# Kernel optimization log

Measured on AMD Instinct MI355X. Metric: run time of the kernel, lower is better.

The kernel has to match this reference:

```python
import jax, jax.numpy as jnp
import numpy as np
from jax import lax

B, T, HID, NH = 4, 2048, 1024, 16
D = HID // NH
LN_EPS = 1e-5
NORM_EPS = 1e-6


def setup_inputs() -> dict:
    key = jax.random.key(0)
    ks = jax.random.split(key, 3)
    s = 0.02
    return {
        "x": jax.random.normal(ks[0], (B, T, HID), jnp.float32),
        "ln_g": jnp.ones((HID,), jnp.float32),
        "ln_b": jnp.zeros((HID,), jnp.float32),
        "w_qkvb": jax.random.normal(ks[1], (HID, 4 * HID), jnp.float32) * s,
        "b_qkvb": jnp.zeros((4 * HID,), jnp.float32),
        "w_out": jax.random.normal(ks[2], (HID, HID), jnp.float32) * s,
        "b_out": jnp.zeros((HID,), jnp.float32),
    }


def reference(x, ln_g, ln_b, w_qkvb, b_qkvb, w_out, b_out):
    b, t = x.shape[:2]
    # LayerNorm (biased variance, eps=1e-5, matching nn.LayerNorm)
    mu = jnp.mean(x, axis=-1, keepdims=True)
    var = jnp.mean((x - mu) ** 2, axis=-1, keepdims=True)
    normed = (x - mu) * lax.rsqrt(var + LN_EPS) * ln_g + ln_b

    proj = normed @ w_qkvb + b_qkvb  # [B,T,4H]
    q, k, v, beta_pre = jnp.split(proj, 4, axis=-1)
    beta = jax.nn.sigmoid(beta_pre)

    def heads(a):  # [B,T,H] -> [T,B,NH,D] (time-major for scan)
        return a.reshape(b, t, NH, D).transpose(1, 0, 2, 3)

    q, k, v, beta = heads(q), heads(k), heads(v), heads(beta)
    # F.normalize(k, dim=-1, eps=1e-6)
    k = k / jnp.maximum(jnp.linalg.norm(k, axis=-1, keepdims=True), NORM_EPS)

    S0 = jnp.zeros((b, NH, D, D), x.dtype)

    def step(S, inp):
        q_t, k_t, v_t, beta_t = inp  # each [B,NH,D]
        retrieval = jnp.einsum('bhij,bhj->bhi', S, k_t)
        S = S + jnp.einsum('bhi,bhj->bhij', beta_t * (v_t - retrieval), k_t)
        o_t = jnp.einsum('bhij,bhj->bhi', S, q_t)
        return S, o_t

    _, out_t = lax.scan(step, S0, (q, k, v, beta))  # out_t: [T,B,NH,D]
    scan_out = out_t.transpose(1, 0, 2, 3).reshape(b, t, NH * D)
    return x + scan_out @ w_out + b_out
```

## Files before the change

### kernel.cpp

```cpp
#include <hip/hip_runtime.h>
#include <hip/hip_bf16.h>

typedef __attribute__((ext_vector_type(8))) short short8;
typedef __attribute__((ext_vector_type(4))) float f32x4;

#define P72 72

__device__ __forceinline__ unsigned short f2bf(float f) {
    union { float f; unsigned int u; } v; v.f = f;
    unsigned int r = (v.u + 0x7FFFu + ((v.u >> 16) & 1u)) >> 16;
    return (unsigned short)r;
}
__device__ __forceinline__ float bf2f(unsigned short b) {
    union { unsigned int u; float f; } v; v.u = ((unsigned int)b) << 16; return v.f;
}

#define WAVE_SYNC() do { __asm__ volatile("s_waitcnt lgkmcnt(0)" ::: "memory"); \
                         __builtin_amdgcn_sched_barrier(0); } while (0)

#define LGKM_BARRIER() do { __asm__ volatile("s_waitcnt lgkmcnt(0)" ::: "memory"); \
                            __builtin_amdgcn_s_barrier(); \
                            __builtin_amdgcn_sched_barrier(0); } while (0)

#define ASYNC16(G, L) __builtin_amdgcn_global_load_lds( \
    (const __attribute__((address_space(1))) void*)(G), \
    (__attribute__((address_space(3))) void*)(L), 16, 0, 0)

__global__ __launch_bounds__(256) void ln_wqt_kernel(
    const float* __restrict__ x, const float* __restrict__ g,
    const float* __restrict__ bv_, unsigned short* __restrict__ out,
    const float* __restrict__ w_qkvb, unsigned short* __restrict__ WQT)
{
    __shared__ float pool[32 * 33];
    const int tid = threadIdx.x;
    if (blockIdx.x < 8192) {
        const int row = blockIdx.x;
        const float4 v = ((const float4*)(x + (size_t)row * 1024))[tid];
        float s  = v.x + v.y + v.z + v.w;
        float s2 = v.x * v.x + v.y * v.y + v.z * v.z + v.w * v.w;
#pragma unroll
        for (int off = 1; off < 64; off <<= 1) {
            s  += __shfl_xor(s, off);
            s2 += __shfl_xor(s2, off);
        }
        const int wv = tid >> 6;
        if ((tid & 63) == 0) { pool[wv] = s; pool[4 + wv] = s2; }
        __syncthreads();
        s  = pool[0] + pool[1] + pool[2] + pool[3];
        s2 = pool[4] + pool[5] + pool[6] + pool[7];
        const float mu  = s * (1.0f / 1024.0f);
        const float var = s2 * (1.0f / 1024.0f) - mu * mu;
        const float inv = rsqrtf(var + 1e-5f);
        const float4 gv = ((const float4*)g)[tid];
        const float4 bb = ((const float4*)bv_)[tid];
        ushort4 o;
        o.x = f2bf((v.x - mu) * inv * gv.x + bb.x);
        o.y = f2bf((v.y - mu) * inv * gv.y + bb.y);
        o.z = f2bf((v.z - mu) * inv * gv.z + bb.z);
        o.w = f2bf((v.w - mu) * inv * gv.w + bb.w);
        *(ushort4*)(out + (size_t)row * 1024 + tid * 4) = o;
    } else {
        const int blk = blockIdx.x - 8192;
        const int c0 = (blk & 127) * 32, r0 = (blk >> 7) * 32;
        const int tx = tid & 31, ty = tid >> 5;
#pragma unroll
        for (int yy = 0; yy < 32; yy += 8)
            pool[(ty + yy) * 33 + tx] = w_qkvb[(size_t)(r0 + ty + yy) * 4096 + c0 + tx];
        __syncthreads();
#pragma unroll
        for (int yy = 0; yy < 32; yy += 8)
            WQT[(size_t)(c0 + ty + yy) * 1024 + r0 + tx] = f2bf(pool[tx * 33 + ty + yy]);
    }
}

__global__ __launch_bounds__(256) void gemm128(
    const unsigned short* __restrict__ A, const unsigned short* __restrict__ Bt,
    const float* __restrict__ bias, int K, int N, int mode, int n0_off,
    const float* __restrict__ resid, float* __restrict__ outf,
    unsigned short* __restrict__ qo, unsigned short* __restrict__ ko,
    unsigned short* __restrict__ vo, unsigned short* __restrict__ bo)
{
    __shared__ __align__(16) unsigned short SMEM[24576];
    const int tid = threadIdx.x;
    const int nwg = (int)(gridDim.x * gridDim.y);
    const int flat = (int)(blockIdx.y * gridDim.x + blockIdx.x);
    const int id2 = (flat & 7) * (nwg >> 3) + (flat >> 3);
    const int M0 = (id2 / (int)gridDim.x) * 128;
    const int N0 = (id2 % (int)gridDim.x) * 128 + n0_off;
    const int lane = tid & 63;
    const int w = tid >> 6, wr = w >> 1, wc = w & 1;
    const int r15 = lane & 15, kg = lane >> 4;
    const int lr = lane >> 2, lc = (lane & 3) * 8;

    const unsigned short* Arow0 = A  + (size_t)(M0 + w * 16 + lr) * K + lc;
    const unsigned short* Arow1 = A  + (size_t)(M0 + 64 + w * 16 + lr) * K + lc;
    const unsigned short* Brow0 = Bt + (size_t)(N0 + w * 16 + lr) * K + lc;
    const unsigned short* Brow1 = Bt + (size_t)(N0 + 64 + w * 16 + lr) * K + lc;

    f32x4 acc[4][4] = {};

    ASYNC16(Arow0, &SMEM[(w * 16) * 32]);
    ASYNC16(Arow1, &SMEM[(64 + w * 16) * 32]);
    ASYNC16(Brow0, &SMEM[12288 + (w * 16) * 32]);
    ASYNC16(Brow1, &SMEM[12288 + (64 + w * 16) * 32]);
    if (32 < K) {
        ASYNC16(Arow0 + 32, &SMEM[4096 + (w * 16) * 32]);
        ASYNC16(Arow1 + 32, &SMEM[4096 + (64 + w * 16) * 32]);
        ASYNC16(Brow0 + 32, &SMEM[12288 + 4096 + (w * 16) * 32]);
        ASYNC16(Brow1 + 32, &SMEM[12288 + 4096 + (64 + w * 16) * 32]);
    }

    int cur = 0;
    for (int k0 = 0; k0 < K; k0 += 32) {
        if (k0 + 64 < K) {
            int n2 = cur + 2; if (n2 >= 3) n2 -= 3;
            const int nb = n2 * 4096;
            ASYNC16(Arow0 + k0 + 64, &SMEM[nb + (w * 16) * 32]);
            ASYNC16(Arow1 + k0 + 64, &SMEM[nb + (64 + w * 16) * 32]);
            ASYNC16(Brow0 + k0 + 64, &SMEM[12288 + nb + (w * 16) * 32]);
            ASYNC16(Brow1 + k0 + 64, &SMEM[12288 + nb + (64 + w * 16) * 32]);
            __asm__ volatile("s_waitcnt vmcnt(8)" ::: "memory");
        } else if (k0 + 32 < K) {
            __asm__ volatile("s_waitcnt vmcnt(4)" ::: "memory");
        } else {
            __asm__ volatile("s_waitcnt vmcnt(0)" ::: "memory");
        }
        __builtin_amdgcn_s_barrier();
        __builtin_amdgcn_sched_barrier(0);
        const int cb = cur * 4096;
        short8 af[4], bf[4];
#pragma unroll
        for (int m = 0; m < 4; m++)
            af[m] = *(const short8*)&SMEM[cb + (wr * 64 + m * 16 + r15) * 32 + kg * 8];
#pragma unroll
        for (int n = 0; n < 4; n++)
            bf[n] = *(const short8*)&SMEM[12288 + cb + (wc * 64 + n * 16 + r15) * 32 + kg * 8];
#pragma unroll
        for (int m = 0; m < 4; m++)
#pragma unroll
            for (int n = 0; n < 4; n++)
                acc[m][n] = __builtin_amdgcn_mfma_f32_16x16x32_bf16(af[m], bf[n], acc[m][n], 0, 0, 0);
        __builtin_amdgcn_sched_barrier(0);
        __builtin_amdgcn_s_barrier();
        cur += 1; if (cur >= 3) cur = 0;
    }

    float bias_r[4];
#pragma unroll
    for (int n = 0; n < 4; n++) bias_r[n] = bias[N0 + wc * 64 + n * 16 + r15];

    if (mode == 0) {
        const int sec = N0 >> 10;
        const int hA = (N0 & 1023) >> 6;
        unsigned short* arr = (sec == 0) ? qo : (sec == 1) ? ko : (sec == 2) ? vo : bo;
#pragma unroll
        for (int p = 0; p < 2; ++p) {
            __syncthreads();
            if (wr == p) {
#pragma unroll
                for (int m = 0; m < 4; m++)
#pragma unroll
                    for (int n = 0; n < 4; n++)
#pragma unroll
                        for (int j = 0; j < 4; j++) {
                            float val = acc[m][n][j] + bias_r[n];
                            if (sec == 3) val = 1.0f / (1.0f + expf(-val));
                            SMEM[(m * 16 + kg * 4 + j) * 136 + wc * 64 + n * 16 + r15] = f2bf(val);
                        }
            }
            __syncthreads();
            const int tl = tid >> 2, sg = tid & 3;
            const int gm = M0 + p * 64 + tl;
            const int b = gm >> 11, t = gm & 2047;
            const int h = hA + (sg >> 1), d0 = (sg & 1) * 32;
            const int colbase = sg * 32;
            const size_t dst = ((size_t)(b * 16 + h) * 2048 + t) * 64 + d0;
#pragma unroll
            for (int i = 0; i < 4; i++) {
                uint4 v = *(const uint4*)&SMEM[tl * 136 + colbase + i * 8];
                *(uint4*)(arr + dst + i * 8) = v;
            }
        }
    } else {
        float* stf = (float*)SMEM;
#pragma unroll
        for (int p = 0; p < 4; ++p) {
            __syncthreads();
            if (wr == (p >> 1)) {
#pragma unroll
                for (int mm = 0; mm < 2; mm++)
#pragma unroll
                    for (int n = 0; n < 4; n++)
#pragma unroll
                        for (int j = 0; j < 4; j++)
                            stf[(mm * 16 + kg * 4 + j) * 132 + wc * 64 + n * 16 + r15] =
                                acc[(p & 1) * 2 + mm][n][j] + bias_r[n];
            }
            __syncthreads();
            const int rl = tid >> 3, sg = (tid & 7) * 16;
            const size_t rowo = (size_t)(M0 + p * 32 + rl) * N + N0 + sg;
#pragma unroll
            for (int i = 0; i < 4; i++) {
                float4 v = *(const float4*)&stf[rl * 132 + sg + i * 4];
                float4 r = *(const float4*)(resid + rowo + i * 4);
                v.x += r.x; v.y += r.y; v.z += r.z; v.w += r.w;
                *(float4*)(outf + rowo + i * 4) = v;
            }
        }
    }
}

__global__ __launch_bounds__(512, 2) void gemm256(
    const unsigned short* __restrict__ A, const unsigned short* __restrict__ Bt,
    const float* __restrict__ bias, int K, int n0_off,
    unsigned short* __restrict__ qo, unsigned short* __restrict__ ko,
    unsigned short* __restrict__ vo, unsigned short* __restrict__ bo)
{
    __shared__ __align__(16) unsigned short SMEM[73728];
    const int tid = threadIdx.x;
    const int flat = (int)(blockIdx.y * gridDim.x + blockIdx.x);
    const int xcd = flat & 7;
    const int l   = flat >> 3;
    const int grp = l >> 4;
    const int gi  = l & 15;
    const int gM  = grp / 3, gN = grp % 3;
    const int mp  = xcd * 4 + gM * 2 + (gi >> 3);
    const int nt  = gN * 8 + (gi & 7);
    const int M0 = mp * 256;
    const int N0 = nt * 128 + n0_off;

    const int lane = tid & 63, wv = tid >> 6;
    const int wr = wv >> 2, wc = wv & 3;
    const int r15 = lane & 15, kg = lane >> 4;
    const int swz = r15 & 7;

    const int srow = lane >> 3;
    const int schk = (lane & 7) ^ srow;
    const unsigned short* Asrc = A  + (size_t)(M0 + wv * 8 + srow) * K + schk * 8;
    const unsigned short* Bsrc = Bt + (size_t)(N0 + wv * 8 + srow) * K + schk * 8;

    float bias_r[2];
    bias_r[0] = bias[N0 + wc * 32 + r15];
    bias_r[1] = bias[N0 + wc * 32 + 16 + r15];
    __builtin_amdgcn_sched_barrier(0);

    auto stageA = [&](int b_, int ko_, int i_) {
        ASYNC16(Asrc + (size_t)i_ * 64 * K + ko_,
                &SMEM[b_ * 24576 + (i_ * 64 + wv * 8) * 64]);
    };
    auto stageB = [&](int b_, int ko_, int i_) {
        ASYNC16(Bsrc + (size_t)i_ * 64 * K + ko_,
                &SMEM[b_ * 24576 + 16384 + (i_ * 64 + wv * 8) * 64]);
    };

#pragma unroll
    for (int i = 0; i < 4; i++) stageA(0, 0, i);
    stageB(0, 0, 0); stageB(0, 0, 1);
#pragma unroll
    for (int i = 0; i < 4; i++) stageA(1, 64, i);
    stageB(1, 64, 0); stageB(1, 64, 1);

    f32x4 acc[8][2] = {};

#define PH_PRE() do { __builtin_amdgcn_s_barrier(); \
                      __asm__ volatile("s_waitcnt lgkmcnt(0)" ::: "memory"); \
                      __builtin_amdgcn_sched_barrier(0); \
                      __builtin_amdgcn_s_setprio(1); } while (0)
#define PH_POST() do { __builtin_amdgcn_s_setprio(0); \
                       __builtin_amdgcn_sched_barrier(0); \
                       __builtin_amdgcn_s_barrier(); } while (0)

    const int NT = K >> 6;
    int cur = 0;
    for (int t = 0; t < NT; ++t) {
        if (t + 1 < NT) { __asm__ volatile("s_waitcnt vmcnt(6)" ::: "memory"); }
        else            { __asm__ volatile("s_waitcnt vmcnt(0)" ::: "memory"); }
        __builtin_amdgcn_s_barrier();
        __builtin_amdgcn_sched_barrier(0);

        const unsigned short* Ab = &SMEM[cur * 24576];
        const unsigned short* Bb = &SMEM[cur * 24576 + 16384];
        int nb = cur + 2; if (nb >= 3) nb -= 3;
        const int nko = (t + 2) * 64;
        const bool pf = (t + 2 < NT);

        short8 af[4], bf[2];
#pragma unroll
        for (int m = 0; m < 4; m++)
            af[m] = *(const short8*)&Ab[(wr * 128 + m * 16 + r15) * 64 + (kg ^ swz) * 8];
#pragma unroll
        for (int n = 0; n < 2; n++)
            bf[n] = *(const short8*)&Bb[(wc * 32 + n * 16 + r15) * 64 + (kg ^ swz) * 8];
        if (pf) { stageA(nb, nko, 0); stageA(nb, nko, 1); }
        PH_PRE();
#pragma unroll
        for (int m = 0; m < 4; m++)
#pragma unroll
            for (int n = 0; n < 2; n++)
                acc[m][n] = __builtin_amdgcn_mfma_f32_16x16x32_bf16(af[m], bf[n], acc[m][n], 0, 0, 0);
        PH_POST();
#pragma unroll
        for (int m = 0; m < 4; m++)
            af[m] = *(const short8*)&Ab[(wr * 128 + (m + 4) * 16 + r15) * 64 + (kg ^ swz) * 8];
        if (pf) { stageA(nb, nko, 2); stageA(nb, nko, 3); }
        PH_PRE();
#pragma unroll
        for (int m = 0; m < 4; m++)
#pragma unroll
            for (int n = 0; n < 2; n++)
                acc[m + 4][n] = __builtin_amdgcn_mfma_f32_16x16x32_bf16(af[m], bf[n], acc[m + 4][n], 0, 0, 0);
        PH_POST();
#pragma unroll
        for (int m = 0; m < 4; m++)
            af[m] = *(const short8*)&Ab[(wr * 128 + m * 16 + r15) * 64 + ((4 + kg) ^ swz) * 8];
#pragma unroll
        for (int n = 0; n < 2; n++)
            bf[n] = *(const short8*)&Bb[(wc * 32 + n * 16 + r15) * 64 + ((4 + kg) ^ swz) * 8];
        if (pf) { stageB(nb, nko, 0); stageB(nb, nko, 1); }
        PH_PRE();
#pragma unroll
        for (int m = 0; m < 4; m++)
#pragma unroll
            for (int n = 0; n < 2; n++)
                acc[m][n] = __builtin_amdgcn_mfma_f32_16x16x32_bf16(af[m], bf[n], acc[m][n], 0, 0, 0);
        PH_POST();
#pragma unroll
        for (int m = 0; m < 4; m++)
            af[m] = *(const short8*)&Ab[(wr * 128 + (m + 4) * 16 + r15) * 64 + ((4 + kg) ^ swz) * 8];
        PH_PRE();
#pragma unroll
        for (int m = 0; m < 4; m++)
#pragma unroll
            for (int n = 0; n < 2; n++)
                acc[m + 4][n] = __builtin_amdgcn_mfma_f32_16x16x32_bf16(af[m], bf[n], acc[m + 4][n], 0, 0, 0);
        __builtin_amdgcn_s_setprio(0);
        __builtin_amdgcn_sched_barrier(0);

        cur += 1; if (cur >= 3) cur = 0;
    }
#undef PH_PRE
#undef PH_POST

    const int sec = N0 >> 10;
    const int hA = (N0 & 1023) >> 6;
    unsigned short* arr = (sec == 0) ? qo : (sec == 1) ? ko : (sec == 2) ? vo : bo;
#pragma unroll
    for (int p = 0; p < 2; ++p) {
        __syncthreads();
        if (wr == p) {
#pragma unroll
            for (int m = 0; m < 8; m++)
#pragma unroll
                for (int n = 0; n < 2; n++)
#pragma unroll
                    for (int j = 0; j < 4; j++) {
                        float val = acc[m][n][j] + bias_r[n];
                        if (sec == 3) val = 1.0f / (1.0f + expf(-val));
                        SMEM[(m * 16 + kg * 4 + j) * 136 + wc * 32 + n * 16 + r15] = f2bf(val);
                    }
        }
        __syncthreads();
        const int row = tid >> 2, sg = tid & 3;
        const int gm = M0 + p * 128 + row;
        const int b = gm >> 11, tt = gm & 2047;
        const int h = hA + (sg >> 1), d0 = (sg & 1) * 32;
        const size_t dst = ((size_t)(b * 16 + h) * 2048 + tt) * 64 + d0;
#pragma unroll
        for (int i = 0; i < 4; i++) {
            uint4 v = *(const uint4*)&SMEM[row * 136 + sg * 32 + i * 8];
            *(uint4*)(arr + dst + i * 8) = v;
        }
    }
}

__global__ __launch_bounds__(256) void prep_kernel(
    const unsigned short* __restrict__ Kpre, const unsigned short* __restrict__ Vin,
    const unsigned short* __restrict__ Bin,
    unsigned short* __restrict__ Kb, unsigned short* __restrict__ A0g,
    float* __restrict__ A0Dg, unsigned short* __restrict__ KTg,
    unsigned short* __restrict__ VTg, unsigned short* __restrict__ BTg)
{
    __shared__ __align__(16) unsigned short Ks[64 * P72];
    __shared__ __align__(16) unsigned short Vs[64 * P72];
    __shared__ __align__(16) unsigned short Bs[64 * P72];
    __shared__ __align__(16) unsigned short Os[64 * P72];
    const int cid = blockIdx.x, tid = threadIdx.x;
    const size_t gbase = (size_t)cid * 4096;
    const int r0 = tid >> 2, c0 = (tid & 3) * 16;
    {
        uint4 k0 = *(const uint4*)(Kpre + gbase + r0 * 64 + c0), k1 = *(const uint4*)(Kpre + gbase + r0 * 64 + c0 + 8);
        uint4 v0 = *(const uint4*)(Vin + gbase + r0 * 64 + c0),  v1 = *(const uint4*)(Vin + gbase + r0 * 64 + c0 + 8);
        uint4 b0 = *(const uint4*)(Bin + gbase + r0 * 64 + c0),  b1 = *(const uint4*)(Bin + gbase + r0 * 64 + c0 + 8);
        *(uint4*)&Ks[r0 * P72 + c0] = k0; *(uint4*)&Ks[r0 * P72 + c0 + 8] = k1;
        *(uint4*)&Vs[r0 * P72 + c0] = v0; *(uint4*)&Vs[r0 * P72 + c0 + 8] = v1;
        *(uint4*)&Bs[r0 * P72 + c0] = b0; *(uint4*)&Bs[r0 * P72 + c0 + 8] = b1;
    }
    __syncthreads();
    {
        const int row = tid >> 2, seg = tid & 3;
        float v[16]; float ss = 0.f;
#pragma unroll
        for (int q = 0; q < 16; q++) { v[q] = bf2f(Ks[row * P72 + seg * 16 + q]); ss = fmaf(v[q], v[q], ss); }
        ss += __shfl_xor(ss, 1); ss += __shfl_xor(ss, 2);
        const float inv = 1.0f / fmaxf(sqrtf(ss), 1e-6f);
        unsigned short t16[16];
#pragma unroll
        for (int q = 0; q < 16; q++) t16[q] = f2bf(v[q] * inv);
        *(uint4*)&Ks[row * P72 + seg * 16]     = *(uint4*)&t16[0];
        *(uint4*)&Ks[row * P72 + seg * 16 + 8] = *(uint4*)&t16[8];
        *(uint4*)(Kb + gbase + row * 64 + seg * 16)     = *(uint4*)&t16[0];
        *(uint4*)(Kb + gbase + row * 64 + seg * 16 + 8) = *(uint4*)&t16[8];
    }
    __syncthreads();
    const int lane = tid & 63, w = tid >> 6;
    const int r15 = lane & 15, kg = lane >> 4;
    f32x4 acc[4] = {{0,0,0,0},{0,0,0,0},{0,0,0,0},{0,0,0,0}};
#pragma unroll
    for (int ks = 0; ks < 2; ks++) {
        short8 afr = *(const short8*)&Ks[(w * 16 + r15) * P72 + ks * 32 + kg * 8];
#pragma unroll
        for (int n = 0; n < 4; n++) {
            short8 bfr = *(const short8*)&Ks[(n * 16 + r15) * P72 + ks * 32 + kg * 8];
            acc[n] = __builtin_amdgcn_mfma_f32_16x16x32_bf16(afr, bfr, acc[n], 0, 0, 0);
        }
    }
#pragma unroll
    for (int n = 0; n < 4; n++) {
#pragma unroll
        for (int j = 0; j < 4; j++) {
            const int s = w * 16 + kg * 4 + j, r = n * 16 + r15;
            Os[s * P72 + r] = (r < s) ? f2bf(acc[n][j]) : (unsigned short)0;
        }
        if (n == w) {
            float4 d;
            d.x = (r15 < kg * 4 + 0) ? acc[n][0] : 0.f;
            d.y = (r15 < kg * 4 + 1) ? acc[n][1] : 0.f;
            d.z = (r15 < kg * 4 + 2) ? acc[n][2] : 0.f;
            d.w = (r15 < kg * 4 + 3) ? acc[n][3] : 0.f;
            *(float4*)(A0Dg + (size_t)cid * 1024 + w * 256 + r15 * 16 + kg * 4) = d;
        }
    }
    __syncthreads();
    {
        uint4 x0 = *(const uint4*)&Os[r0 * P72 + c0];
        uint4 x1 = *(const uint4*)&Os[r0 * P72 + c0 + 8];
        *(uint4*)(A0g + gbase + r0 * 64 + c0) = x0;
        *(uint4*)(A0g + gbase + r0 * 64 + c0 + 8) = x1;
    }
    {
        const int d = tid >> 2, s0 = (tid & 3) * 16;
        unsigned short tk[16], tv[16], tb[16];
#pragma unroll
        for (int k = 0; k < 16; k++) {
            tk[k] = Ks[(s0 + k) * P72 + d];
            tv[k] = Vs[(s0 + k) * P72 + d];
            tb[k] = Bs[(s0 + k) * P72 + d];
        }
        *(uint4*)(KTg + gbase + (size_t)d * 64 + s0)     = *(uint4*)&tk[0];
        *(uint4*)(KTg + gbase + (size_t)d * 64 + s0 + 8) = *(uint4*)&tk[8];
        *(uint4*)(VTg + gbase + (size_t)d * 64 + s0)     = *(uint4*)&tv[0];
        *(uint4*)(VTg + gbase + (size_t)d * 64 + s0 + 8) = *(uint4*)&tv[8];
        *(uint4*)(BTg + gbase + (size_t)d * 64 + s0)     = *(uint4*)&tb[0];
        *(uint4*)(BTg + gbase + (size_t)d * 64 + s0 + 8) = *(uint4*)&tb[8];
    }
}

__global__ __launch_bounds__(256, 1) void fused_scan_kernel(
    const unsigned short* __restrict__ A0g, const unsigned short* __restrict__ Kb,
    const unsigned short* __restrict__ KTg, const float* __restrict__ A0Dg,
    const unsigned short* __restrict__ VTg, const unsigned short* __restrict__ BTg,
    unsigned short* __restrict__ Scg, unsigned short* __restrict__ UTg,
    const unsigned short* __restrict__ NORM, const unsigned short* __restrict__ WQT,
    const float* __restrict__ bias, unsigned short* __restrict__ qo,
    const float* __restrict__ w_out, unsigned short* __restrict__ WOT)
{
    __shared__ __align__(16) unsigned char POOL[120832];
    unsigned short* us = (unsigned short*)POOL;
    const int tid = threadIdx.x;

    if (blockIdx.x < 64) {
        unsigned short* sK  = us;
        unsigned short* sKT = us + 9216;
        unsigned short* sA0 = us + 18432;
        unsigned short* sVT = us + 27648;
        unsigned short* sBT = us + 36864;
        float* sA0D = (float*)(POOL + 92160);
        unsigned short* Sbf = us + 51200;
        unsigned short* UTs = us + 55808;

        const int bh = blockIdx.x;
        const int lane = tid & 63, w = tid >> 6;
        const int r15 = lane & 15, kg = lane >> 4;
        const int sr = tid >> 2, sc = (tid & 3) * 16;
        const int qr = 16 * w + (lane >> 2), qc = (lane & 3) * 16;
        const size_t base0 = (size_t)bh * 32 * 4096;
        const size_t baseD = (size_t)bh * 32 * 1024;
        const int dOff = (w * 16 + (sr & 15)) * 20 + (tid & 3) * 4;

        f32x4 Sreg[4] = {};
        uint4 g[10]; float4 gD;

        const uint4 z4 = {0u, 0u, 0u, 0u};
        *(uint4*)&Sbf[sr * P72 + sc] = z4;
        *(uint4*)&Sbf[sr * P72 + sc + 8] = z4;
        {
            const size_t gb = base0 + sr * 64 + sc;
            g[0] = *(const uint4*)(Kb  + gb); g[1] = *(const uint4*)(Kb  + gb + 8);
            g[2] = *(const uint4*)(KTg + gb); g[3] = *(const uint4*)(KTg + gb + 8);
            g[4] = *(const uint4*)(A0g + gb); g[5] = *(const uint4*)(A0g + gb + 8);
            g[6] = *(const uint4*)(VTg + gb); g[7] = *(const uint4*)(VTg + gb + 8);
            g[8] = *(const uint4*)(BTg + gb); g[9] = *(const uint4*)(BTg + gb + 8);
            gD   = *(const float4*)(A0Dg + baseD + tid * 4);
            *(uint4*)&sK [sr * P72 + sc] = g[0]; *(uint4*)&sK [sr * P72 + sc + 8] = g[1];
            *(uint4*)&sKT[sr * P72 + sc] = g[2]; *(uint4*)&sKT[sr * P72 + sc + 8] = g[3];
            *(uint4*)&sA0[sr * P72 + sc] = g[4]; *(uint4*)&sA0[sr * P72 + sc + 8] = g[5];
            *(uint4*)&sVT[sr * P72 + sc] = g[6]; *(uint4*)&sVT[sr * P72 + sc + 8] = g[7];
            *(uint4*)&sBT[sr * P72 + sc] = g[8]; *(uint4*)&sBT[sr * P72 + sc + 8] = g[9];
            *(float4*)&sA0D[dOff] = gD;
        }

#pragma unroll 1
        for (int c = 0; c < 32; ++c) {
            const int cur = c & 1, nxt = cur ^ 1;
            LGKM_BARRIER();
            if (c < 31) {
                const size_t gb = base0 + (size_t)(c + 1) * 4096 + sr * 64 + sc;
                g[0] = *(const uint4*)(Kb  + gb); g[1] = *(const uint4*)(Kb  + gb + 8);
                g[2] = *(const uint4*)(KTg + gb); g[3] = *(const uint4*)(KTg + gb + 8);
                g[4] = *(const uint4*)(A0g + gb); g[5] = *(const uint4*)(A0g + gb + 8);
                g[6] = *(const uint4*)(VTg + gb); g[7] = *(const uint4*)(VTg + gb + 8);
                g[8] = *(const uint4*)(BTg + gb); g[9] = *(const uint4*)(BTg + gb + 8);
                gD   = *(const float4*)(A0Dg + baseD + (size_t)(c + 1) * 1024 + tid * 4);
            }
            const unsigned short* KsC  = &sK [cur * 4608];
            const unsigned short* KTsC = &sKT[cur * 4608];
            const unsigned short* A0C  = &sA0[cur * 4608];
            const unsigned short* VTC  = &sVT[cur * 4608];
            const unsigned short* BTC  = &sBT[cur * 4608];
            const float*          A0DC = &sA0D[cur * 1280];

            *(uint4*)&UTs[(16 * w + r15) * P72 + kg * 16] = z4;
            *(uint4*)&UTs[(16 * w + r15) * P72 + kg * 16 + 8] = z4;

            {
                uint4 a = *(const uint4*)&Sbf[qr * P72 + qc];
                uint4 b2 = *(const uint4*)&Sbf[qr * P72 + qc + 8];
                const unsigned FL = 0x80008000u;
                a.x ^= FL; a.y ^= FL; a.z ^= FL; a.w ^= FL;
                b2.x ^= FL; b2.y ^= FL; b2.z ^= FL; b2.w ^= FL;
                const size_t so = base0 + (size_t)c * 4096 + qr * 64 + qc;
                *(uint4*)(Scg + so) = a;
                *(uint4*)(Scg + so + 8) = b2;
            }

            f32x4 y[4];
#pragma unroll
            for (int st = 0; st < 4; st++) {
                ushort4 vv = *(const ushort4*)&VTC[(16 * w + r15) * P72 + st * 16 + kg * 4];
                y[st][0] = bf2f(vv.x); y[st][1] = bf2f(vv.y);
                y[st][2] = bf2f(vv.z); y[st][3] = bf2f(vv.w);
            }
#pragma unroll
            for (int ks = 0; ks < 2; ks++) {
                short8 bfr = *(const short8*)&Sbf[(16 * w + r15) * P72 + ks * 32 + kg * 8];
#pragma unroll
                for (int st = 0; st < 4; st++) {
                    short8 afr = *(const short8*)&KsC[(st * 16 + r15) * P72 + ks * 32 + kg * 8];
                    y[st] = __builtin_amdgcn_mfma_f32_16x16x32_bf16(afr, bfr, y[st], 0, 0, 0);
                }
            }

#pragma unroll
            for (int b = 0; b < 4; b++) {
                if (b > 0) {
                    WAVE_SYNC();
                    f32x4 corr = {};
                    {
                        short8 afr = *(const short8*)&A0C[(b * 16 + r15) * P72 + kg * 8];
                        short8 bfr = *(const short8*)&UTs[(16 * w + r15) * P72 + kg * 8];
                        corr = __builtin_amdgcn_mfma_f32_16x16x32_bf16(afr, bfr, corr, 0, 0, 0);
                    }
                    if (b == 3) {
                        short8 afr = *(const short8*)&A0C[(b * 16 + r15) * P72 + 32 + kg * 8];
                        short8 bfr = *(const short8*)&UTs[(16 * w + r15) * P72 + 32 + kg * 8];
                        corr = __builtin_amdgcn_mfma_f32_16x16x32_bf16(afr, bfr, corr, 0, 0, 0);
                    }
                    y[b] = y[b] - corr;
                }
                ushort4 bt4 = *(const ushort4*)&BTC[(16 * w + r15) * P72 + b * 16 + kg * 4];
                const float bta0 = bf2f(bt4.x), bta1 = bf2f(bt4.y);
                const float bta2 = bf2f(bt4.z), bta3 = bf2f(bt4.w);
                float us0 = 0.f, us1 = 0.f, us2 = 0.f, us3 = 0.f;
#pragma unroll
                for (int own = 0; own < 4; own++) {
                    const f32x4 c40 = *(const f32x4*)&A0DC[(b * 16 + own * 4 + 0) * 20 + kg * 4];
                    const f32x4 c41 = *(const f32x4*)&A0DC[(b * 16 + own * 4 + 1) * 20 + kg * 4];
                    const f32x4 c42 = *(const f32x4*)&A0DC[(b * 16 + own * 4 + 2) * 20 + kg * 4];
                    const f32x4 c43 = *(const f32x4*)&A0DC[(b * 16 + own * 4 + 3) * 20 + kg * 4];
                    if (kg == own) {
                        us0 = bta0 * y[b][0];
                        us1 = bta1 * (y[b][1] - c40[1] * us0);
                        us2 = bta2 * (y[b][2] - c40[2] * us0 - c41[2] * us1);
                        us3 = bta3 * (y[b][3] - c40[3] * us0 - c41[3] * us1 - c42[3] * us2);
                    }
                    const int src = own * 16 + r15;
                    const float u0 = __shfl(us0, src), u1 = __shfl(us1, src);
                    const float u2 = __shfl(us2, src), u3 = __shfl(us3, src);
                    if (kg > own)
                        y[b] = y[b] - (c40 * u0 + c41 * u1 + c42 * u2 + c43 * u3);
                }
                ushort4 up;
                up.x = f2bf(us0); up.y = f2bf(us1); up.z = f2bf(us2); up.w = f2bf(us3);
                *(ushort4*)&UTs[(16 * w + r15) * P72 + b * 16 + kg * 4] = up;
            }
            WAVE_SYNC();

            {
                uint4 a = *(const uint4*)&UTs[qr * P72 + qc];
                uint4 b2 = *(const uint4*)&UTs[qr * P72 + qc + 8];
                const size_t so = base0 + (size_t)c * 4096 + qr * 64 + qc;
                *(uint4*)(UTg + so) = a;
                *(uint4*)(UTg + so + 8) = b2;
            }

#pragma unroll
            for (int ks = 0; ks < 2; ks++) {
                short8 afr = *(const short8*)&UTs[(16 * w + r15) * P72 + ks * 32 + kg * 8];
#pragma unroll
                for (int n = 0; n < 4; n++) {
                    short8 bfr = *(const short8*)&KTsC[(n * 16 + r15) * P72 + ks * 32 + kg * 8];
                    Sreg[n] = __builtin_amdgcn_mfma_f32_16x16x32_bf16(afr, bfr, Sreg[n], 0, 0, 0);
                }
            }
#pragma unroll
            for (int n = 0; n < 4; n++)
#pragma unroll
                for (int jj = 0; jj < 4; jj++)
                    Sbf[(16 * w + kg * 4 + jj) * P72 + n * 16 + r15] = f2bf(-Sreg[n][jj]);

            if (c < 31) {
                *(uint4*)&sK [nxt * 4608 + sr * P72 + sc] = g[0]; *(uint4*)&sK [nxt * 4608 + sr * P72 + sc + 8] = g[1];
                *(uint4*)&sKT[nxt * 4608 + sr * P72 + sc] = g[2]; *(uint4*)&sKT[nxt * 4608 + sr * P72 + sc + 8] = g[3];
                *(uint4*)&sA0[nxt * 4608 + sr * P72 + sc] = g[4]; *(uint4*)&sA0[nxt * 4608 + sr * P72 + sc + 8] = g[5];
                *(uint4*)&sVT[nxt * 4608 + sr * P72 + sc] = g[6]; *(uint4*)&sVT[nxt * 4608 + sr * P72 + sc + 8] = g[7];
                *(uint4*)&sBT[nxt * 4608 + sr * P72 + sc] = g[8]; *(uint4*)&sBT[nxt * 4608 + sr * P72 + sc + 8] = g[9];
                *(float4*)&sA0D[nxt * 1280 + dOff] = gD;
            }
        }
    } else if (blockIdx.x < 64 + 512) {
        unsigned short* SMEM = us;
        const int blk = blockIdx.x - 64;
        const int id2 = (blk & 7) * 64 + (blk >> 3);
        const int M0 = (id2 >> 3) * 128, N0 = (id2 & 7) * 128;
        const int K = 1024;
        const int lane = tid & 63;
        const int w = tid >> 6, wr = w >> 1, wc = w & 1;
        const int r15 = lane & 15, kg = lane >> 4;
        const int lr = lane >> 2, lc = (lane & 3) * 8;

        const unsigned short* Arow0 = NORM + (size_t)(M0 + w * 16 + lr) * K + lc;
        const unsigned short* Arow1 = NORM + (size_t)(M0 + 64 + w * 16 + lr) * K + lc;
        const unsigned short* Brow0 = WQT + (size_t)(N0 + w * 16 + lr) * K + lc;
        const unsigned short* Brow1 = WQT + (size_t)(N0 + 64 + w * 16 + lr) * K + lc;

        f32x4 acc[4][4] = {};

        ASYNC16(Arow0, &SMEM[(w * 16) * 32]);
        ASYNC16(Arow1, &SMEM[(64 + w * 16) * 32]);
        ASYNC16(Brow0, &SMEM[8192 + (w * 16) * 32]);
        ASYNC16(Brow1, &SMEM[8192 + (64 + w * 16) * 32]);

        int cur = 0;
        for (int k0 = 0; k0 < K; k0 += 32) {
            if (k0 + 32 < K) {
                const int nb = (cur ^ 1) * 4096;
                ASYNC16(Arow0 + k0 + 32, &SMEM[nb + (w * 16) * 32]);
                ASYNC16(Arow1 + k0 + 32, &SMEM[nb + (64 + w * 16) * 32]);
                ASYNC16(Brow0 + k0 + 32, &SMEM[8192 + nb + (w * 16) * 32]);
                ASYNC16(Brow1 + k0 + 32, &SMEM[8192 + nb + (64 + w * 16) * 32]);
                __asm__ volatile("s_waitcnt vmcnt(4)" ::: "memory");
            } else {
                __asm__ volatile("s_waitcnt vmcnt(0)" ::: "memory");
            }
            __builtin_amdgcn_s_barrier();
            __builtin_amdgcn_sched_barrier(0);
            const int cb = cur * 4096;
            short8 af[4], bf[4];
#pragma unroll
            for (int m = 0; m < 4; m++)
                af[m] = *(const short8*)&SMEM[cb + (wr * 64 + m * 16 + r15) * 32 + kg * 8];
#pragma unroll
            for (int n = 0; n < 4; n++)
                bf[n] = *(const short8*)&SMEM[8192 + cb + (wc * 64 + n * 16 + r15) * 32 + kg * 8];
#pragma unroll
            for (int m = 0; m < 4; m++)
#pragma unroll
                for (int n = 0; n < 4; n++)
                    acc[m][n] = __builtin_amdgcn_mfma_f32_16x16x32_bf16(af[m], bf[n], acc[m][n], 0, 0, 0);
            __builtin_amdgcn_sched_barrier(0);
            __builtin_amdgcn_s_barrier();
            cur ^= 1;
        }

        float bias_r[4];
#pragma unroll
        for (int n = 0; n < 4; n++) bias_r[n] = bias[N0 + wc * 64 + n * 16 + r15];
        const int hA = N0 >> 6;
#pragma unroll
        for (int p = 0; p < 2; ++p) {
            __syncthreads();
            if (wr == p) {
#pragma unroll
                for (int m = 0; m < 4; m++)
#pragma unroll
                    for (int n = 0; n < 4; n++)
#pragma unroll
                        for (int j = 0; j < 4; j++)
                            SMEM[(m * 16 + kg * 4 + j) * 136 + wc * 64 + n * 16 + r15] =
                                f2bf(acc[m][n][j] + bias_r[n]);
            }
            __syncthreads();
            const int tl = tid >> 2, sg = tid & 3;
            const int gm = M0 + p * 64 + tl;
            const int b = gm >> 11, t = gm & 2047;
            const int h = hA + (sg >> 1), d0 = (sg & 1) * 32;
            const int colbase = sg * 32;
            const size_t dst = ((size_t)(b * 16 + h) * 2048 + t) * 64 + d0;
#pragma unroll
            for (int i = 0; i < 4; i++) {
                uint4 v = *(const uint4*)&SMEM[tl * 136 + colbase + i * 8];
                *(uint4*)(qo + dst + i * 8) = v;
            }
        }
    } else {
        float* tile = (float*)POOL;
        const int blk = blockIdx.x - 64 - 512;
        const int c0 = (blk & 31) * 32, r0 = (blk >> 5) * 32;
        const int tx = tid & 31, ty = tid >> 5;
#pragma unroll
        for (int yy = 0; yy < 32; yy += 8)
            tile[(ty + yy) * 33 + tx] = w_out[(size_t)(r0 + ty + yy) * 1024 + c0 + tx];
        __syncthreads();
#pragma unroll
        for (int yy = 0; yy < 32; yy += 8)
            WOT[(size_t)(c0 + ty + yy) * 1024 + r0 + tx] = f2bf(tile[tx * 33 + ty + yy]);
    }
}

__global__ __launch_bounds__(256) void out_kernel(
    const unsigned short* __restrict__ Qb, const unsigned short* __restrict__ Kb,
    const unsigned short* __restrict__ Scg, const unsigned short* __restrict__ UTg,
    unsigned short* __restrict__ attn)
{
    __shared__ __align__(16) unsigned short Qs[64 * P72];
    __shared__ __align__(16) unsigned short Kbs[64 * P72];
    __shared__ __align__(16) unsigned short Scs[64 * P72];
    __shared__ __align__(16) unsigned short UTss[64 * P72];
    __shared__ __align__(16) unsigned short Ms[64 * P72];
    __shared__ __align__(16) unsigned short Osb[64 * P72];
    const int blk = blockIdx.x, tid = threadIdx.x;
    const int bh = blk >> 5, cc = blk & 31;
    const size_t gbase = (size_t)blk * 4096;
    const int lane = tid & 63, w = tid >> 6;
    const int r15 = lane & 15, kg = lane >> 4;
    {
        const int r0 = tid >> 2, c0 = (tid & 3) * 16;
        uint4 q0 = *(const uint4*)(Qb + gbase + r0 * 64 + c0),  q1 = *(const uint4*)(Qb + gbase + r0 * 64 + c0 + 8);
        uint4 k0 = *(const uint4*)(Kb + gbase + r0 * 64 + c0),  k1 = *(const uint4*)(Kb + gbase + r0 * 64 + c0 + 8);
        uint4 s0 = *(const uint4*)(Scg + gbase + r0 * 64 + c0), s1 = *(const uint4*)(Scg + gbase + r0 * 64 + c0 + 8);
        uint4 u0 = *(const uint4*)(UTg + gbase + r0 * 64 + c0), u1 = *(const uint4*)(UTg + gbase + r0 * 64 + c0 + 8);
        *(uint4*)&Qs [r0 * P72 + c0] = q0; *(uint4*)&Qs [r0 * P72 + c0 + 8] = q1;
        *(uint4*)&Kbs[r0 * P72 + c0] = k0; *(uint4*)&Kbs[r0 * P72 + c0 + 8] = k1;
        *(uint4*)&Scs[r0 * P72 + c0] = s0; *(uint4*)&Scs[r0 * P72 + c0 + 8] = s1;
        *(uint4*)&UTss[r0 * P72 + c0] = u0; *(uint4*)&UTss[r0 * P72 + c0 + 8] = u1;
    }
    __syncthreads();
    {
        f32x4 accm[4] = {{0,0,0,0},{0,0,0,0},{0,0,0,0},{0,0,0,0}};
#pragma unroll
        for (int ks = 0; ks < 2; ks++) {
            short8 afr = *(const short8*)&Qs[(w * 16 + r15) * P72 + ks * 32 + kg * 8];
#pragma unroll
            for (int n = 0; n < 4; n++) {
                short8 bfr = *(const short8*)&Kbs[(n * 16 + r15) * P72 + ks * 32 + kg * 8];
                accm[n] = __builtin_amdgcn_mfma_f32_16x16x32_bf16(afr, bfr, accm[n], 0, 0, 0);
            }
        }
#pragma unroll
        for (int n = 0; n < 4; n++)
#pragma unroll
            for (int j = 0; j < 4; j++) {
                const int t = w * 16 + kg * 4 + j, s = n * 16 + r15;
                Ms[t * P72 + s] = (s <= t) ? f2bf(accm[n][j]) : (unsigned short)0;
            }
    }
    __syncthreads();
    {
        f32x4 acc[4] = {{0,0,0,0},{0,0,0,0},{0,0,0,0},{0,0,0,0}};
#pragma unroll
        for (int ks = 0; ks < 2; ks++) {
            short8 afr = *(const short8*)&Qs[(w * 16 + r15) * P72 + ks * 32 + kg * 8];
#pragma unroll
            for (int n = 0; n < 4; n++) {
                short8 bfr = *(const short8*)&Scs[(n * 16 + r15) * P72 + ks * 32 + kg * 8];
                acc[n] = __builtin_amdgcn_mfma_f32_16x16x32_bf16(afr, bfr, acc[n], 0, 0, 0);
            }
        }
#pragma unroll
        for (int ks = 0; ks < 2; ks++) {
            short8 afr = *(const short8*)&Ms[(w * 16 + r15) * P72 + ks * 32 + kg * 8];
#pragma unroll
            for (int n = 0; n < 4; n++) {
                short8 bfr = *(const short8*)&UTss[(n * 16 + r15) * P72 + ks * 32 + kg * 8];
                acc[n] = __builtin_amdgcn_mfma_f32_16x16x32_bf16(afr, bfr, acc[n], 0, 0, 0);
            }
        }
#pragma unroll
        for (int n = 0; n < 4; n++)
#pragma unroll
            for (int j = 0; j < 4; j++) {
                const int t = w * 16 + kg * 4 + j, i = n * 16 + r15;
                Osb[t * P72 + i] = f2bf(acc[n][j]);
            }
    }
    __syncthreads();
    {
        const int b = bh >> 4, h = bh & 15;
        const int t = tid >> 2, i0 = (tid & 3) * 16;
        uint4 o0 = *(const uint4*)&Osb[t * P72 + i0];
        uint4 o1 = *(const uint4*)&Osb[t * P72 + i0 + 8];
        unsigned short* dst = attn + ((size_t)(b * 2048 + cc * 64 + t)) * 1024 + h * 64 + i0;
        *(uint4*)dst = o0;
        *(uint4*)(dst + 8) = o1;
    }
}

extern "C" void kernel_launch(void* const* d_in, const int* in_sizes, int n_in,
                              void* d_out, int out_size, void* d_ws, size_t ws_size,
                              hipStream_t stream)
{
    const float* x      = (const float*)d_in[0];
    const float* ln_g   = (const float*)d_in[1];
    const float* ln_b   = (const float*)d_in[2];
    const float* w_qkvb = (const float*)d_in[3];
    const float* b_qkvb = (const float*)d_in[4];
    const float* w_out  = (const float*)d_in[5];
    const float* b_out  = (const float*)d_in[6];
    float* out = (float*)d_out;

    char* ws = (char*)d_ws;
    size_t off = 0;
    auto alloc = [&](size_t bytes) -> char* {
        char* p = ws + off;
        off = (off + bytes + 255) & ~(size_t)255;
        return p;
    };
    const size_t TOK = 64ull * 2048 * 64;
    unsigned short* WQT  = (unsigned short*)alloc(4096ull * 1024 * 2);
    unsigned short* WOT  = (unsigned short*)alloc(1024ull * 1024 * 2);
    unsigned short* NORM = (unsigned short*)alloc(TOK * 2 * 2);
    unsigned short* Qb   = (unsigned short*)alloc(TOK * 2);
    unsigned short* Kpre = (unsigned short*)alloc(TOK * 2);
    unsigned short* Kb   = (unsigned short*)alloc(TOK * 2);
    unsigned short* KTb  = (unsigned short*)alloc(TOK * 2);
    unsigned short* Vb   = (unsigned short*)alloc(TOK * 2);
    unsigned short* Bb   = (unsigned short*)alloc(TOK * 2);
    unsigned short* A0   = (unsigned short*)alloc(TOK * 2);
    unsigned short* Sc   = (unsigned short*)alloc(TOK * 2);
    unsigned short* UT   = (unsigned short*)alloc(TOK * 2);
    float*          A0D  = (float*)alloc(2048ull * 1024 * 4);
    unsigned short* ATTN = NORM;
    unsigned short* VTb  = Vb;
    unsigned short* BTb  = Bb;

    hipLaunchKernelGGL(ln_wqt_kernel, dim3(8192 + 4096), dim3(256), 0, stream,
                       x, ln_g, ln_b, NORM, w_qkvb, WQT);
    hipLaunchKernelGGL(gemm256, dim3(24, 32), dim3(512), 0, stream,
                       NORM, WQT, b_qkvb, 1024, 1024, Qb, Kpre, Vb, Bb);
    hipLaunchKernelGGL(prep_kernel, dim3(2048), dim3(256), 0, stream,
                       Kpre, Vb, Bb, Kb, A0, A0D, KTb, VTb, BTb);
    hipLaunchKernelGGL(fused_scan_kernel, dim3(64 + 512 + 1024), dim3(256), 0, stream,
                       A0, Kb, KTb, A0D, VTb, BTb, Sc, UT,
                       NORM, WQT, b_qkvb, Qb, w_out, WOT);
    hipLaunchKernelGGL(out_kernel, dim3(2048), dim3(256), 0, stream, Qb, Kb, Sc, UT, ATTN);
    hipLaunchKernelGGL(gemm128, dim3(8, 64), dim3(256), 0, stream,
                       ATTN, WOT, b_out, 1024, 1024, 1, 0,
                       x, out, (unsigned short*)nullptr, (unsigned short*)nullptr,
                       (unsigned short*)nullptr, (unsigned short*)nullptr);
}
```

Baseline: 318.3 us.

## Pre-tile and swizzle GEMM operands so async LDS loads read contiguous blocks

The LayerNorm/weight-transpose kernel now also writes tiled, XOR-swizzled copies of the normalized activations and the transposed QKV weights, laid out as contiguous 256x64 and 128x64 tiles. The main QKV GEMM stages these tiles with fully contiguous 16-byte global-to-LDS loads instead of strided row loads. The aim is better global-load coalescing and simpler address math in the GEMM. The cost is extra global writes and workspace for the duplicate buffers, plus a scattered 2-byte store pattern in the weight transpose.

```diff
diff --git a/kernel.cpp b/kernel.cpp
--- a/kernel.cpp
+++ b/kernel.cpp
@@ -29,7 +29,8 @@
 __global__ __launch_bounds__(256) void ln_wqt_kernel(
     const float* __restrict__ x, const float* __restrict__ g,
     const float* __restrict__ bv_, unsigned short* __restrict__ out,
-    const float* __restrict__ w_qkvb, unsigned short* __restrict__ WQT)
+    const float* __restrict__ w_qkvb, unsigned short* __restrict__ WQT,
+    unsigned short* __restrict__ NORMT, unsigned short* __restrict__ WQTT)
 {
     __shared__ float pool[32 * 33];
     const int tid = threadIdx.x;
@@ -59,6 +60,12 @@
         o.z = f2bf((v.z - mu) * inv * gv.z + bb.z);
         o.w = f2bf((v.w - mu) * inv * gv.w + bb.w);
         *(ushort4*)(out + (size_t)row * 1024 + tid * 4) = o;
+        {
+            const int r  = row & 255;
+            const int t  = (row >> 8) * 16 + (tid >> 4);
+            const int sc = ((tid >> 1) & 7) ^ (r & 7);
+            *(ushort4*)(NORMT + (size_t)t * 16384 + r * 64 + sc * 8 + (tid & 1) * 4) = o;
+        }
     } else {
         const int blk = blockIdx.x - 8192;
         const int c0 = (blk & 127) * 32, r0 = (blk >> 7) * 32;
@@ -67,9 +74,16 @@
         for (int yy = 0; yy < 32; yy += 8)
             pool[(ty + yy) * 33 + tx] = w_qkvb[(size_t)(r0 + ty + yy) * 4096 + c0 + tx];
         __syncthreads();
-#pragma unroll
-        for (int yy = 0; yy < 32; yy += 8)
-            WQT[(size_t)(c0 + ty + yy) * 1024 + r0 + tx] = f2bf(pool[tx * 33 + ty + yy]);
+        const int k = r0 + tx;
+#pragma unroll
+        for (int yy = 0; yy < 32; yy += 8) {
+            const int n = c0 + ty + yy;
+            const unsigned short val = f2bf(pool[tx * 33 + ty + yy]);
+            WQT[(size_t)n * 1024 + k] = val;
+            const int sc = (((k & 63) >> 3) ^ (n & 7));
+            WQTT[((size_t)(n >> 7) * 16 + (k >> 6)) * 8192 +
+                 (n & 127) * 64 + sc * 8 + (k & 7)] = val;
+        }
     }
 }
 
@@ -234,31 +248,26 @@
     const int r15 = lane & 15, kg = lane >> 4;
     const int swz = r15 & 7;
 
-    const int srow = lane >> 3;
-    const int schk = (lane & 7) ^ srow;
-    const unsigned short* Asrc = A  + (size_t)(M0 + wv * 8 + srow) * K + schk * 8;
-    const unsigned short* Bsrc = Bt + (size_t)(N0 + wv * 8 + srow) * K + schk * 8;
-
     float bias_r[2];
     bias_r[0] = bias[N0 + wc * 32 + r15];
     bias_r[1] = bias[N0 + wc * 32 + 16 + r15];
     __builtin_amdgcn_sched_barrier(0);
 
-    auto stageA = [&](int b_, int ko_, int i_) {
-        ASYNC16(Asrc + (size_t)i_ * 64 * K + ko_,
-                &SMEM[b_ * 24576 + (i_ * 64 + wv * 8) * 64]);
+    auto stageA = [&](int b_, int kt_, int i_) {
+        ASYNC16(A + ((size_t)(M0 >> 8) * 16 + kt_) * 16384 + (wv * 4 + i_) * 512 + lane * 8,
+                &SMEM[b_ * 24576 + (wv * 4 + i_) * 512]);
     };
-    auto stageB = [&](int b_, int ko_, int i_) {
-        ASYNC16(Bsrc + (size_t)i_ * 64 * K + ko_,
-                &SMEM[b_ * 24576 + 16384 + (i_ * 64 + wv * 8) * 64]);
+    auto stageB = [&](int b_, int kt_, int i_) {
+        ASYNC16(Bt + ((size_t)(N0 >> 7) * 16 + kt_) * 8192 + (wv * 2 + i_) * 512 + lane * 8,
+                &SMEM[b_ * 24576 + 16384 + (wv * 2 + i_) * 512]);
     };
 
 #pragma unroll
     for (int i = 0; i < 4; i++) stageA(0, 0, i);
     stageB(0, 0, 0); stageB(0, 0, 1);
 #pragma unroll
-    for (int i = 0; i < 4; i++) stageA(1, 64, i);
-    stageB(1, 64, 0); stageB(1, 64, 1);
+    for (int i = 0; i < 4; i++) stageA(1, 1, i);
+    stageB(1, 1, 0); stageB(1, 1, 1);
 
     f32x4 acc[8][2] = {};
 
@@ -281,7 +290,7 @@
         const unsigned short* Ab = &SMEM[cur * 24576];
         const unsigned short* Bb = &SMEM[cur * 24576 + 16384];
         int nb = cur + 2; if (nb >= 3) nb -= 3;
-        const int nko = (t + 2) * 64;
+        const int nkt = t + 2;
         const bool pf = (t + 2 < NT);
 
         short8 af[4], bf[2];
@@ -291,7 +300,7 @@
 #pragma unroll
         for (int n = 0; n < 2; n++)
             bf[n] = *(const short8*)&Bb[(wc * 32 + n * 16 + r15) * 64 + (kg ^ swz) * 8];
-        if (pf) { stageA(nb, nko, 0); stageA(nb, nko, 1); }
+        if (pf) { stageA(nb, nkt, 0); stageA(nb, nkt, 1); }
         PH_PRE();
 #pragma unroll
         for (int m = 0; m < 4; m++)
@@ -302,7 +311,7 @@
 #pragma unroll
         for (int m = 0; m < 4; m++)
             af[m] = *(const short8*)&Ab[(wr * 128 + (m + 4) * 16 + r15) * 64 + (kg ^ swz) * 8];
-        if (pf) { stageA(nb, nko, 2); stageA(nb, nko, 3); }
+        if (pf) { stageA(nb, nkt, 2); stageA(nb, nkt, 3); }
         PH_PRE();
 #pragma unroll
         for (int m = 0; m < 4; m++)
@@ -316,7 +325,7 @@
 #pragma unroll
         for (int n = 0; n < 2; n++)
             bf[n] = *(const short8*)&Bb[(wc * 32 + n * 16 + r15) * 64 + ((4 + kg) ^ swz) * 8];
-        if (pf) { stageB(nb, nko, 0); stageB(nb, nko, 1); }
+        if (pf) { stageB(nb, nkt, 0); stageB(nb, nkt, 1); }
         PH_PRE();
 #pragma unroll
         for (int m = 0; m < 4; m++)
@@ -857,8 +866,10 @@
     };
     const size_t TOK = 64ull * 2048 * 64;
     unsigned short* WQT  = (unsigned short*)alloc(4096ull * 1024 * 2);
+    unsigned short* WQTT = (unsigned short*)alloc(4096ull * 1024 * 2);
     unsigned short* WOT  = (unsigned short*)alloc(1024ull * 1024 * 2);
     unsigned short* NORM = (unsigned short*)alloc(TOK * 2 * 2);
+    unsigned short* NORMT= (unsigned short*)alloc(TOK * 2 * 2);
     unsigned short* Qb   = (unsigned short*)alloc(TOK * 2);
     unsigned short* Kpre = (unsigned short*)alloc(TOK * 2);
     unsigned short* Kb   = (unsigned short*)alloc(TOK * 2);
@@ -874,9 +885,9 @@
     unsigned short* BTb  = Bb;
 
     hipLaunchKernelGGL(ln_wqt_kernel, dim3(8192 + 4096), dim3(256), 0, stream,
-                       x, ln_g, ln_b, NORM, w_qkvb, WQT);
+                       x, ln_g, ln_b, NORM, w_qkvb, WQT, NORMT, WQTT);
     hipLaunchKernelGGL(gemm256, dim3(24, 32), dim3(512), 0, stream,
-                       NORM, WQT, b_qkvb, 1024, 1024, Qb, Kpre, Vb, Bb);
+                       NORMT, WQTT, b_qkvb, 1024, 1024, Qb, Kpre, Vb, Bb);
     hipLaunchKernelGGL(prep_kernel, dim3(2048), dim3(256), 0, stream,
                        Kpre, Vb, Bb, Kb, A0, A0D, KTb, VTb, BTb);
     hipLaunchKernelGGL(fused_scan_kernel, dim3(64 + 512 + 1024), dim3(256), 0, stream,
```

Result: no change. 323.1 us (+1.5%).
